# Kernel optimization log

Hardware: AMD Instinct MI355X
Metric: run time of the kernel (lower is better)

Reference implementation:

```python
import jax, jax.numpy as jnp
import numpy as np

B, P, H = 256, 20, 4  # images, boxes per image, humans per image
F, L, S, HD, C = 1024, 300, 16, 1024, 117

def _build_edges():
    s, d = np.meshgrid(np.arange(P), np.arange(P), indexing='ij')
    m = s != d
    src_l, dst_l = s[m], d[m]  # 380 fully-connected edges per image (src-major order)
    eid_tab = -np.ones((P, P), np.int64)
    eid_tab[src_l, dst_l] = np.arange(src_l.shape[0])
    rs, rd = np.meshgrid(np.arange(P), np.arange(H), indexing='ij')
    rm = rs != rd
    r_eid = eid_tab[rs[rm], rd[rm]]  # 76 readout edges per image (human dst)
    off_n = (np.arange(B) * P)[:, None]
    off_e = (np.arange(B) * src_l.shape[0])[:, None]
    edge_src = (src_l[None] + off_n).ravel().astype(np.int32)
    edge_dst = (dst_l[None] + off_n).ravel().astype(np.int32)
    readout_eid = (r_eid[None] + off_e).ravel().astype(np.int32)
    return edge_src, edge_dst, readout_eid

def setup_inputs() -> dict:
    key = jax.random.key(0)
    ks = jax.random.split(key, 12)
    es, ed, re = _build_edges()
    N = B * P
    D_in = 2 * F + 2 * L + S  # 2664
    return {
        'feat': jax.random.normal(ks[0], (N, F), jnp.float32),
        'word2vec': jax.random.normal(ks[1], (N, L), jnp.float32),
        'spatial_feat': jax.random.normal(ks[2], (es.shape[0], S), jnp.float32),
        'W_v': jax.random.normal(ks[3], (F, F), jnp.float32) / np.float32(np.sqrt(F)),
        'a_v': jax.random.normal(ks[4], (2 * F,), jnp.float32) * 0.05,
        'W_l': jax.random.normal(ks[5], (L, L), jnp.float32) / np.float32(np.sqrt(L)),
        'a_l': jax.random.normal(ks[6], (2 * L,), jnp.float32) * 0.05,
        'W1': jax.random.normal(ks[7], (D_in, HD), jnp.float32) / np.float32(np.sqrt(D_in)),
        'b1': jnp.zeros((HD,), jnp.float32),
        'W2': jax.random.normal(ks[8], (HD, C), jnp.float32) / np.float32(np.sqrt(HD)),
        'b2': jnp.zeros((C,), jnp.float32),
        'edge_src': jnp.asarray(es),
        'edge_dst': jnp.asarray(ed),
        'readout_eid': jnp.asarray(re),
    }

def _gat_update(x, W, a, src, dst, n):
    # graph-attention message passing (GRNN step): attention over incoming edges per dst
    h = x @ W                      # [N, d]
    d = h.shape[1]
    e_src = h @ a[:d]              # [N]
    e_dst = h @ a[d:]
    e = jax.nn.leaky_relu(e_src[src] + e_dst[dst], 0.2)          # [E]
    emax = jax.ops.segment_max(e, dst, num_segments=n)
    ee = jnp.exp(e - emax[dst])
    denom = jax.ops.segment_sum(ee, dst, num_segments=n)
    alpha = ee / (denom[dst] + 1e-9)                              # segment softmax
    msg = jax.ops.segment_sum(alpha[:, None] * h[src], dst, num_segments=n)  # [N, d]
    return jax.nn.relu(x + msg)

def reference(feat, word2vec, spatial_feat, W_v, a_v, W_l, a_l, W1, b1, W2, b2,
              edge_src, edge_dst, readout_eid):
    n = feat.shape[0]
    new_n_f = _gat_update(feat, W_v, a_v, edge_src, edge_dst, n)          # visual stream
    new_n_f_lang = _gat_update(word2vec, W_l, a_l, edge_src, edge_dst, n) # semantic stream
    s = edge_src[readout_eid]
    d = edge_dst[readout_eid]
    s_f = spatial_feat[readout_eid]
    # Predictor.forward: concat [dst visual, dst lang, edge spatial, src lang, src visual]
    x = jnp.concatenate([new_n_f[d], new_n_f_lang[d], s_f, new_n_f_lang[s], new_n_f[s]], axis=1)
    hdn = jax.nn.relu(x @ W1 + b1)
    return hdn @ W2 + b2  # [Er, 117] action logits
```

## Files before the change

### kernel.cpp

```cpp
#include <hip/hip_runtime.h>
#include <hip/hip_bf16.h>

#define BB 256
#define PP 20
#define HH 4
#define FF 1024
#define LL 300
#define LLP 320
#define DCAT 1344
#define SS 16
#define HDIM 1024
#define CC 117
#define NNODE (BB * PP)
#define NREAD (BB * (PP * HH - HH))
#define EPB 8
#define TK 32

typedef __attribute__((ext_vector_type(8))) short bf16x8v;
typedef __attribute__((ext_vector_type(4))) float f32x4v;
typedef __attribute__((ext_vector_type(4))) unsigned short u16x4;

__device__ __forceinline__ float bf2f(unsigned short u) {
  return __uint_as_float((unsigned int)u << 16);
}
__device__ __forceinline__ unsigned short f2b(float f) {
  __hip_bfloat16 h = __float2bfloat16(f);
  return *(unsigned short*)&h;
}

__global__ void sniff_dtype(const unsigned short* __restrict__ buf,
                            int* __restrict__ flag) {
  int t = threadIdx.x;
  int votes = 0;
  for (int i = t; i < 512; i += 256) {
    unsigned int u = (unsigned int)buf[i] << 16;
    float v = __uint_as_float(u);
    float a = fabsf(v);
    if (v == v && a > 9.3e-10f && a < 1.1e9f) votes++;
  }
  __shared__ int sv[256];
  sv[t] = votes;
  __syncthreads();
  for (int s = 128; s > 0; s >>= 1) {
    if (t < s) sv[t] += sv[t + s];
    __syncthreads();
  }
  if (t == 0) flag[0] = (sv[0] < 448) ? 1 : 0;
}

#define NB_FEAT 5120
#define NB_W2V 1600
#define NB_SM 79
#define PREP_BLOCKS 10739

__global__ __launch_bounds__(256) void prep_all(
    const void* __restrict__ s0, const void* __restrict__ s1,
    const void* __restrict__ s3, const void* __restrict__ s4,
    const void* __restrict__ s5, const void* __restrict__ s6,
    const void* __restrict__ s7, const void* __restrict__ s8,
    const void* __restrict__ s9, const void* __restrict__ s10,
    __hip_bfloat16* __restrict__ xcat, __hip_bfloat16* __restrict__ cAv,
    __hip_bfloat16* __restrict__ cAl, __hip_bfloat16* __restrict__ cB1,
    __hip_bfloat16* __restrict__ cB2, __hip_bfloat16* __restrict__ cW1sp,
    __hip_bfloat16* __restrict__ dWvT, __hip_bfloat16* __restrict__ dWlT,
    __hip_bfloat16* __restrict__ dW1d, __hip_bfloat16* __restrict__ dW1s,
    __hip_bfloat16* __restrict__ dW2T, const int* __restrict__ flag) {
  const int bid = blockIdx.x;
  const int t = threadIdx.x;
  const int fl = flag[0];

  if (bid < NB_FEAT) {
    long i = (long)bid * 256 + t;
    int r = (int)(i >> 8);
    int c = ((int)i & 255) * 4;
    u16x4 o;
    if (fl) {
      float4 v = *(const float4*)((const float*)s0 + (long)r * FF + c);
      o[0] = f2b(v.x); o[1] = f2b(v.y); o[2] = f2b(v.z); o[3] = f2b(v.w);
    } else {
      o = *(const u16x4*)((const __hip_bfloat16*)s0 + (long)r * FF + c);
    }
    *(u16x4*)(xcat + (long)r * DCAT + c) = o;
  } else if (bid < NB_FEAT + NB_W2V) {
    long i = (long)(bid - NB_FEAT) * 256 + t;
    int r = (int)(i / 80), c = ((int)(i % 80)) * 4;
    u16x4 o;
    if (c + 4 <= LL) {
      if (fl) {
        const float* p = (const float*)s1 + (long)r * LL + c;
        o[0] = f2b(p[0]); o[1] = f2b(p[1]); o[2] = f2b(p[2]); o[3] = f2b(p[3]);
      } else {
        const __hip_bfloat16* p = (const __hip_bfloat16*)s1 + (long)r * LL + c;
        o[0] = *(const unsigned short*)(p + 0);
        o[1] = *(const unsigned short*)(p + 1);
        o[2] = *(const unsigned short*)(p + 2);
        o[3] = *(const unsigned short*)(p + 3);
      }
    } else {
#pragma unroll
      for (int j = 0; j < 4; j++) {
        float v = 0.f;
        if (c + j < LL)
          v = fl ? ((const float*)s1)[(long)r * LL + c + j]
                 : __bfloat162float(
                       ((const __hip_bfloat16*)s1)[(long)r * LL + c + j]);
        o[j] = f2b(v);
      }
    }
    *(u16x4*)(xcat + (long)r * DCAT + FF + c) = o;
  } else if (bid < NB_FEAT + NB_W2V + NB_SM) {
    int i = (bid - NB_FEAT - NB_W2V) * 256 + t;
    auto rd = [&](const void* p, long idx) -> float {
      return fl ? ((const float*)p)[idx]
                : __bfloat162float(((const __hip_bfloat16*)p)[idx]);
    };
    if (i < 2048) cAv[i] = __float2bfloat16(rd(s4, i));
    else if (i < 2648) cAl[i - 2048] = __float2bfloat16(rd(s6, i - 2048));
    else if (i < 3672) cB1[i - 2648] = __float2bfloat16(rd(s8, i - 2648));
    else if (i < 3789) cB2[i - 3672] = __float2bfloat16(rd(s10, i - 3672));
    else if (i < 20173)
      cW1sp[i - 3789] = __float2bfloat16(rd(s7, 1355776L + (i - 3789)));
  } else {
    int idx = bid - (NB_FEAT + NB_W2V + NB_SM);
    const int OFFS[8] = {0, 1024, 1124, 2148, 2468, 3492, 3812, 3940};
    const int NKB[7] = {32, 10, 32, 10, 32, 10, 32};
    const int ROW0[7] = {0, 0, 0, 1024, 1640, 1340, 0};
    const int KK[7] = {1024, 300, 1024, 300, 1024, 300, 1024};
    const int NN[7] = {1024, 300, 1024, 1024, 1024, 1024, 117};
    const int LD[7] = {1024, 300, 1024, 1024, 1024, 1024, 117};
    const int KP[7] = {1024, 320, 1024, 320, 1024, 320, 1024};
    const int KOFF[7] = {0, 0, 0, 1024, 0, 1024, 0};
    const int KLD[7] = {1024, 320, DCAT, DCAT, DCAT, DCAT, 1024};
    int z = 0;
    while (z < 6 && idx >= OFFS[z + 1]) z++;
    idx -= OFFS[z];
    const int kb = (idx % NKB[z]) * 32, nb = (idx / NKB[z]) * 32;
    const void* src = (z == 0) ? s3 : (z == 1) ? s5 : (z == 6) ? s9 : s7;
    __hip_bfloat16* dst = (z == 0) ? dWvT : (z == 1) ? dWlT
                          : (z <= 3) ? dW1d : (z <= 5) ? dW1s : dW2T;
    const int row0 = ROW0[z], K = KK[z], N = NN[z], ld = LD[z], Kp = KP[z];
    const int koff = KOFF[z], kld = KLD[z];
    __shared__ float tile[32][33];
    const int tx = t & 31, ty = t >> 5;
    for (int i = ty; i < 32; i += 8) {
      int k = kb + i, n = nb + tx;
      float v = 0.f;
      if (k < K && n < N) {
        long sidx = (long)(row0 + k) * ld + n;
        v = fl ? ((const float*)src)[sidx]
               : __bfloat162float(((const __hip_bfloat16*)src)[sidx]);
      }
      tile[i][tx] = v;
    }
    __syncthreads();
    for (int i = ty; i < 32; i += 8) {
      int n = nb + i, k = kb + tx;
      if (n < N && k < Kp)
        dst[(long)n * kld + koff + k] = __float2bfloat16(tile[tx][i]);
    }
  }
}

struct GDesc {
  const __hip_bfloat16* A;
  const __hip_bfloat16* BT;
  void* C;
  const __hip_bfloat16* bias;
  int M, N, K, lda, ldbt, ldc;
  int row_mode, do_relu, c_mode, nbx, nby;
};

template <int BM, int BN, int WR, int WC>
__global__ __launch_bounds__(256) void gemm_db(GDesc d0, GDesc d1,
                                               const int* outflag) {
  constexpr int MI = BM / WR / 16;
  constexpr int NI = BN / WC / 16;
  __shared__ __hip_bfloat16 Asm[2][BM * TK];
  __shared__ __hip_bfloat16 Bsm[2][BN * TK];
  const GDesc d = blockIdx.z ? d1 : d0;
  if ((int)blockIdx.x >= d.nbx || (int)blockIdx.y >= d.nby) return;
  const int tid = threadIdx.x;
  const int lane = tid & 63;
  const int wave = tid >> 6;
  const int wm = (wave % WR) * (BM / WR);
  const int wn = (wave / WR) * (BN / WC);
  const int m0 = blockIdx.y * BM;
  const int n0 = blockIdx.x * BN;
  const int col_l = lane & 15;
  const int quad = lane >> 4;
  const __hip_bfloat16* A = d.A;
  const __hip_bfloat16* BT = d.BT;
  const int M = d.M, N = d.N, lda = d.lda, ldbt = d.ldbt;
  const int row_mode = d.row_mode;

  auto stage = [&](int k0, int buf) {
#pragma unroll
    for (int c = tid; c < BM * 4; c += 256) {
      int r = c >> 2;
      int koff = (c & 3) * 8;
      int row = m0 + r;
      if (row >= M) row = M - 1;
      long grow = row_mode ? ((long)(row >> 2) * PP + (row & 3)) : (long)row;
      const __hip_bfloat16* gp = A + grow * lda + k0 + koff;
      __builtin_amdgcn_global_load_lds(
          (const __attribute__((address_space(1))) unsigned int*)gp,
          (__attribute__((address_space(3))) unsigned int*)(&Asm[buf][c * 8]),
          16, 0, 0);
    }
#pragma unroll
    for (int c = tid; c < BN * 4; c += 256) {
      int r = c >> 2;
      int koff = (c & 3) * 8;
      int row = n0 + r;
      if (row >= N) row = N - 1;
      const __hip_bfloat16* gp = BT + (long)row * ldbt + k0 + koff;
      __builtin_amdgcn_global_load_lds(
          (const __attribute__((address_space(1))) unsigned int*)gp,
          (__attribute__((address_space(3))) unsigned int*)(&Bsm[buf][c * 8]),
          16, 0, 0);
    }
  };

  f32x4v acc[MI][NI];
#pragma unroll
  for (int i = 0; i < MI; i++)
#pragma unroll
    for (int j = 0; j < NI; j++)
#pragma unroll
      for (int r = 0; r < 4; r++) acc[i][j][r] = 0.f;

  const int nk = d.K / TK;
  stage(0, 0);
  __syncthreads();
  for (int kt = 0; kt < nk; kt++) {
    const int cur = kt & 1;
    if (kt + 1 < nk) stage((kt + 1) * TK, 1 - cur);
    bf16x8v af[MI], bfr[NI];
#pragma unroll
    for (int mi = 0; mi < MI; mi++)
      af[mi] =
          *(const bf16x8v*)&Asm[cur][(wm + mi * 16 + col_l) * TK + quad * 8];
#pragma unroll
    for (int ni = 0; ni < NI; ni++)
      bfr[ni] =
          *(const bf16x8v*)&Bsm[cur][(wn + ni * 16 + col_l) * TK + quad * 8];
#pragma unroll
    for (int mi = 0; mi < MI; mi++)
#pragma unroll
      for (int ni = 0; ni < NI; ni++)
        acc[mi][ni] = __builtin_amdgcn_mfma_f32_16x16x32_bf16(
            af[mi], bfr[ni], acc[mi][ni], 0, 0, 0);
    __syncthreads();
  }

  const int store_f32 =
      (d.c_mode == 1) || (d.c_mode == 2 && outflag && outflag[0]);
#pragma unroll
  for (int mi = 0; mi < MI; mi++) {
    int rbase = m0 + wm + mi * 16 + quad * 4;
#pragma unroll
    for (int ni = 0; ni < NI; ni++) {
      int col = n0 + wn + ni * 16 + col_l;
      if (col >= N) continue;
      float bv = d.bias ? __bfloat162float(d.bias[col]) : 0.f;
#pragma unroll
      for (int r = 0; r < 4; r++) {
        int row = rbase + r;
        if (row >= M) continue;
        float v = acc[mi][ni][r] + bv;
        if (d.do_relu) v = fmaxf(v, 0.f);
        if (store_f32)
          ((float*)d.C)[(long)row * d.ldc + col] = v;
        else
          ((__hip_bfloat16*)d.C)[(long)row * d.ldc + col] = __float2bfloat16(v);
      }
    }
  }
}

#define CHROW (DCAT / 4)

__global__ __launch_bounds__(1024) void attn_fused(
    const __hip_bfloat16* __restrict__ xcat,
    const __hip_bfloat16* __restrict__ hcat,
    const __hip_bfloat16* __restrict__ aV,
    const __hip_bfloat16* __restrict__ aL,
    __hip_bfloat16* __restrict__ newcat) {
  const int b = blockIdx.x;
  const int t = threadIdx.x;
  const long base = (long)b * PP * DCAT;

  __shared__ __hip_bfloat16 hs[PP][DCAT];
  __shared__ float esv[PP], edv[PP], esl[PP], edl[PP];
  __shared__ float alphaV[PP * PP], alphaL[PP * PP];

  for (int i = t; i < PP * CHROW; i += 1024) {
    int r = i / CHROW, c = (i % CHROW) * 4;
    *(u16x4*)&hs[r][c] = *(const u16x4*)(hcat + base + (long)r * DCAT + c);
  }
  __syncthreads();

  const int wave = t >> 6, lane = t & 63;
  for (int node = wave; node < PP; node += 16) {
    float s1 = 0.f, s2 = 0.f, s3 = 0.f, s4 = 0.f;
    for (int f = lane * 4; f < FF; f += 256) {
      u16x4 hv = *(const u16x4*)&hs[node][f];
      u16x4 a1 = *(const u16x4*)(aV + f);
      u16x4 a2 = *(const u16x4*)(aV + FF + f);
#pragma unroll
      for (int j = 0; j < 4; j++) {
        float hf = bf2f(hv[j]);
        s1 += hf * bf2f(a1[j]);
        s2 += hf * bf2f(a2[j]);
      }
    }
    for (int f = FF + lane * 4; f < FF + LL; f += 256) {
      u16x4 hv = *(const u16x4*)&hs[node][f];
      u16x4 a3 = *(const u16x4*)(aL + (f - FF));
      u16x4 a4 = *(const u16x4*)(aL + LL + (f - FF));
#pragma unroll
      for (int j = 0; j < 4; j++) {
        float hf = bf2f(hv[j]);
        s3 += hf * bf2f(a3[j]);
        s4 += hf * bf2f(a4[j]);
      }
    }
#pragma unroll
    for (int o = 32; o > 0; o >>= 1) {
      s1 += __shfl_down(s1, o);
      s2 += __shfl_down(s2, o);
      s3 += __shfl_down(s3, o);
      s4 += __shfl_down(s4, o);
    }
    if (lane == 0) {
      esv[node] = s1; edv[node] = s2; esl[node] = s3; edl[node] = s4;
    }
  }
  __syncthreads();

  if (t < 2 * PP) {
    const int strm = t / PP, dd = t % PP;
    const float* es = strm ? esl : esv;
    const float ed = strm ? edl[dd] : edv[dd];
    float lg[PP];
    float m = -1e30f;
#pragma unroll
    for (int s = 0; s < PP; s++) {
      float e;
      if (s == dd) e = -1e30f;
      else {
        float v = es[s] + ed;
        e = (v > 0.f) ? v : 0.2f * v;
      }
      lg[s] = e;
      m = fmaxf(m, e);
    }
    float sum = 0.f;
#pragma unroll
    for (int s = 0; s < PP; s++) {
      lg[s] = expf(lg[s] - m);
      sum += lg[s];
    }
    float inv = 1.f / (sum + 1e-9f);
    float* al = strm ? alphaL : alphaV;
#pragma unroll
    for (int s = 0; s < PP; s++) al[s * PP + dd] = lg[s] * inv;
  }
  __syncthreads();

  for (int i = t; i < PP * CHROW; i += 1024) {
    int dd = i / CHROW, c = (i % CHROW) * 4;
    u16x4 ov;
    if (c >= FF + LL) {
      ov[0] = 0; ov[1] = 0; ov[2] = 0; ov[3] = 0;
    } else {
      const float* al = (c < FF) ? (alphaV + dd) : (alphaL + dd);
      float a0 = 0.f, a1 = 0.f, a2 = 0.f, a3 = 0.f;
#pragma unroll
      for (int s = 0; s < PP; s++) {
        float w = al[s * PP];
        u16x4 hv = *(const u16x4*)&hs[s][c];
        a0 += w * bf2f(hv[0]);
        a1 += w * bf2f(hv[1]);
        a2 += w * bf2f(hv[2]);
        a3 += w * bf2f(hv[3]);
      }
      u16x4 xv = *(const u16x4*)(xcat + base + (long)dd * DCAT + c);
      ov[0] = f2b(fmaxf(bf2f(xv[0]) + a0, 0.f));
      ov[1] = f2b(fmaxf(bf2f(xv[1]) + a1, 0.f));
      ov[2] = f2b(fmaxf(bf2f(xv[2]) + a2, 0.f));
      ov[3] = f2b(fmaxf(bf2f(xv[3]) + a3, 0.f));
    }
    *(u16x4*)(newcat + base + (long)dd * DCAT + c) = ov;
  }
}

__global__ __launch_bounds__(256) void combine_kernel(
    const int* __restrict__ e_src, const int* __restrict__ e_dst,
    const int* __restrict__ r_eid, const void* __restrict__ spat_raw,
    const __hip_bfloat16* __restrict__ W1sp,
    const __hip_bfloat16* __restrict__ b1,
    const __hip_bfloat16* __restrict__ Yd, const __hip_bfloat16* __restrict__ Ys,
    __hip_bfloat16* __restrict__ hdn, const int* __restrict__ flag) {
  const int t = threadIdx.x;
  const int e0 = blockIdx.x * EPB;
  const int hd = t * 4;

  float w[SS][4];
#pragma unroll
  for (int k = 0; k < SS; k++) {
    u16x4 ww = *(const u16x4*)(W1sp + (long)k * HDIM + hd);
#pragma unroll
    for (int j = 0; j < 4; j++) w[k][j] = bf2f(ww[j]);
  }
  float bb[4];
  {
    u16x4 bv = *(const u16x4*)(b1 + hd);
#pragma unroll
    for (int j = 0; j < 4; j++) bb[j] = bf2f(bv[j]);
  }

  __shared__ int sh_s[EPB], sh_hx[EPB], sh_re[EPB];
  __shared__ float sh_sf[EPB][SS];
  if (t < EPB) {
    int re = r_eid[e0 + t];
    sh_re[t] = re;
    sh_s[t] = e_src[re];
    int d = e_dst[re];
    sh_hx[t] = (d / PP) * HH + (d % PP);
  }
  __syncthreads();
  if (t < EPB * SS) {
    int ee = t >> 4, k = t & 15;
    long idx = (long)sh_re[ee] * SS + k;
    sh_sf[ee][k] = flag[0]
                       ? ((const float*)spat_raw)[idx]
                       : __bfloat162float(((const __hip_bfloat16*)spat_raw)[idx]);
  }
  __syncthreads();

#pragma unroll
  for (int ee = 0; ee < EPB; ee++) {
    const int s = sh_s[ee];
    const int hx = sh_hx[ee];
    u16x4 yd = *(const u16x4*)(Yd + (long)hx * HDIM + hd);
    u16x4 ys = *(const u16x4*)(Ys + (long)s * HDIM + hd);
    float v[4];
#pragma unroll
    for (int j = 0; j < 4; j++) v[j] = bf2f(yd[j]) + bf2f(ys[j]) + bb[j];
#pragma unroll
    for (int k = 0; k < SS; k++) {
      float sfv = sh_sf[ee][k];
#pragma unroll
      for (int j = 0; j < 4; j++) v[j] += sfv * w[k][j];
    }
    u16x4 o;
#pragma unroll
    for (int j = 0; j < 4; j++) o[j] = f2b(fmaxf(v[j], 0.f));
    *(u16x4*)(hdn + (long)(e0 + ee) * HDIM + hd) = o;
  }
}

extern "C" void kernel_launch(void* const* d_in, const int* in_sizes, int n_in,
                              void* d_out, int out_size, void* d_ws,
                              size_t ws_size, hipStream_t stream) {
  const int* e_src = (const int*)d_in[11];
  const int* e_dst = (const int*)d_in[12];
  const int* r_eid = (const int*)d_in[13];
  (void)ws_size; (void)n_in; (void)in_sizes; (void)out_size;

  char* ws = (char*)d_ws;
  size_t off = 0;
  auto take = [&](size_t bytes) {
    char* p = ws + off;
    off += (bytes + 255) & ~(size_t)255;
    return p;
  };

  int* dflag = (int*)take(256);
  __hip_bfloat16* xcat   = (__hip_bfloat16*)take((size_t)NNODE * DCAT * 2);
  __hip_bfloat16* hcat   = (__hip_bfloat16*)take((size_t)NNODE * DCAT * 2);
  __hip_bfloat16* newcat = (__hip_bfloat16*)take((size_t)NNODE * DCAT * 2);
  __hip_bfloat16* cAv    = (__hip_bfloat16*)take((size_t)2 * FF * 2);
  __hip_bfloat16* cAl    = (__hip_bfloat16*)take((size_t)2 * LL * 2);
  __hip_bfloat16* cB1    = (__hip_bfloat16*)take((size_t)HDIM * 2);
  __hip_bfloat16* cB2    = (__hip_bfloat16*)take((size_t)CC * 2);
  __hip_bfloat16* cW1sp  = (__hip_bfloat16*)take((size_t)SS * HDIM * 2);
  __hip_bfloat16* WvT    = (__hip_bfloat16*)take((size_t)FF * FF * 2);
  __hip_bfloat16* WlT    = (__hip_bfloat16*)take((size_t)LL * LLP * 2);
  __hip_bfloat16* W1Td   = (__hip_bfloat16*)take((size_t)HDIM * DCAT * 2);
  __hip_bfloat16* W1Ts   = (__hip_bfloat16*)take((size_t)HDIM * DCAT * 2);
  __hip_bfloat16* W2T    = (__hip_bfloat16*)take((size_t)CC * HDIM * 2);
  __hip_bfloat16* Yd     = (__hip_bfloat16*)take((size_t)BB * HH * HDIM * 2);
  __hip_bfloat16* Ys     = (__hip_bfloat16*)take((size_t)NNODE * HDIM * 2);
  __hip_bfloat16* hdn    = (__hip_bfloat16*)take((size_t)NREAD * HDIM * 2);

  dim3 blk(256);

  sniff_dtype<<<1, blk, 0, stream>>>((const unsigned short*)d_in[0], dflag);

  prep_all<<<PREP_BLOCKS, blk, 0, stream>>>(
      d_in[0], d_in[1], d_in[3], d_in[4], d_in[5], d_in[6], d_in[7], d_in[8],
      d_in[9], d_in[10], xcat, cAv, cAl, cB1, cB2, cW1sp, WvT, WlT, W1Td, W1Ts,
      W2T, dflag);

  {
    GDesc pv{xcat, WvT, hcat, nullptr,
             NNODE, FF, FF, DCAT, FF, DCAT, 0, 0, 0, 8, 80};
    GDesc pl{xcat + FF, WlT, hcat + FF, nullptr,
             NNODE, LL, LLP, DCAT, LLP, DCAT, 0, 0, 0, 3, 80};
    gemm_db<64, 128, 2, 2><<<dim3(8, 80, 2), blk, 0, stream>>>(pv, pl,
                                                               nullptr);
  }

  attn_fused<<<BB, dim3(1024), 0, stream>>>(xcat, hcat, cAv, cAl, newcat);

  {
    GDesc gys{newcat, W1Ts, Ys, nullptr,
              NNODE, HDIM, DCAT, DCAT, DCAT, HDIM, 0, 0, 0, 8, 80};
    GDesc gyd{newcat, W1Td, Yd, nullptr,
              BB * HH, HDIM, DCAT, DCAT, DCAT, HDIM, 1, 0, 0, 8, 16};
    gemm_db<64, 128, 2, 2><<<dim3(8, 80, 2), blk, 0, stream>>>(gys, gyd,
                                                               nullptr);
  }

  combine_kernel<<<NREAD / EPB, blk, 0, stream>>>(e_src, e_dst, r_eid, d_in[2],
                                                  cW1sp, cB1, Yd, Ys, hdn,
                                                  dflag);

  {
    GDesc go{hdn, W2T, d_out, cB2,
             NREAD, CC, HDIM, HDIM, HDIM, CC, 0, 0, 2, 1, 608};
    gemm_db<32, 128, 1, 4><<<dim3(1, 608, 1), blk, 0, stream>>>(go, go, dflag);
  }
}
```

Baseline: 246.7 us.

## Replace LDS-staged GEMM with direct global-to-register fragment loads

The GEMM kernel no longer stages A/B tiles through double-buffered shared memory with global_load_lds and barriers. Each lane now loads its MFMA fragments straight from global memory into registers, prefetching the next k-step while the current one computes. This removes the LDS traffic and the per-iteration __syncthreads. In exchange, data shared between waves in a block is fetched redundantly from global memory or L2, and each 16-byte load is strided by the row pitch, which may lower coalescing.

Measured after the change: 374.4 us. 1.52x slower.

```diff
diff --git a/kernel.cpp b/kernel.cpp
--- a/kernel.cpp
+++ b/kernel.cpp
@@ -171,12 +171,10 @@
 };
 
 template <int BM, int BN, int WR, int WC>
-__global__ __launch_bounds__(256) void gemm_db(GDesc d0, GDesc d1,
-                                               const int* outflag) {
+__global__ __launch_bounds__(256) void gemm_direct(GDesc d0, GDesc d1,
+                                                   const int* outflag) {
   constexpr int MI = BM / WR / 16;
   constexpr int NI = BN / WC / 16;
-  __shared__ __hip_bfloat16 Asm[2][BM * TK];
-  __shared__ __hip_bfloat16 Bsm[2][BN * TK];
   const GDesc d = blockIdx.z ? d1 : d0;
   if ((int)blockIdx.x >= d.nbx || (int)blockIdx.y >= d.nby) return;
   const int tid = threadIdx.x;
@@ -188,38 +186,23 @@
   const int n0 = blockIdx.x * BN;
   const int col_l = lane & 15;
   const int quad = lane >> 4;
-  const __hip_bfloat16* A = d.A;
-  const __hip_bfloat16* BT = d.BT;
-  const int M = d.M, N = d.N, lda = d.lda, ldbt = d.ldbt;
-  const int row_mode = d.row_mode;
-
-  auto stage = [&](int k0, int buf) {
-#pragma unroll
-    for (int c = tid; c < BM * 4; c += 256) {
-      int r = c >> 2;
-      int koff = (c & 3) * 8;
-      int row = m0 + r;
-      if (row >= M) row = M - 1;
-      long grow = row_mode ? ((long)(row >> 2) * PP + (row & 3)) : (long)row;
-      const __hip_bfloat16* gp = A + grow * lda + k0 + koff;
-      __builtin_amdgcn_global_load_lds(
-          (const __attribute__((address_space(1))) unsigned int*)gp,
-          (__attribute__((address_space(3))) unsigned int*)(&Asm[buf][c * 8]),
-          16, 0, 0);
-    }
-#pragma unroll
-    for (int c = tid; c < BN * 4; c += 256) {
-      int r = c >> 2;
-      int koff = (c & 3) * 8;
-      int row = n0 + r;
-      if (row >= N) row = N - 1;
-      const __hip_bfloat16* gp = BT + (long)row * ldbt + k0 + koff;
-      __builtin_amdgcn_global_load_lds(
-          (const __attribute__((address_space(1))) unsigned int*)gp,
-          (__attribute__((address_space(3))) unsigned int*)(&Bsm[buf][c * 8]),
-          16, 0, 0);
-    }
-  };
+  const int M = d.M, N = d.N;
+
+  const __hip_bfloat16* pA[MI];
+#pragma unroll
+  for (int mi = 0; mi < MI; mi++) {
+    int row = m0 + wm + mi * 16 + col_l;
+    if (row >= M) row = M - 1;
+    long grow = d.row_mode ? ((long)(row >> 2) * PP + (row & 3)) : (long)row;
+    pA[mi] = d.A + grow * d.lda + quad * 8;
+  }
+  const __hip_bfloat16* pB[NI];
+#pragma unroll
+  for (int ni = 0; ni < NI; ni++) {
+    int row = n0 + wn + ni * 16 + col_l;
+    if (row >= N) row = N - 1;
+    pB[ni] = d.BT + (long)row * d.ldbt + quad * 8;
+  }
 
   f32x4v acc[MI][NI];
 #pragma unroll
@@ -230,27 +213,32 @@
       for (int r = 0; r < 4; r++) acc[i][j][r] = 0.f;
 
   const int nk = d.K / TK;
-  stage(0, 0);
-  __syncthreads();
+  bf16x8v afc[MI], bfc[NI], afn[MI], bfn[NI];
+#pragma unroll
+  for (int mi = 0; mi < MI; mi++) afc[mi] = *(const bf16x8v*)(pA[mi]);
+#pragma unroll
+  for (int ni = 0; ni < NI; ni++) bfc[ni] = *(const bf16x8v*)(pB[ni]);
+
   for (int kt = 0; kt < nk; kt++) {
-    const int cur = kt & 1;
-    if (kt + 1 < nk) stage((kt + 1) * TK, 1 - cur);
-    bf16x8v af[MI], bfr[NI];
-#pragma unroll
-    for (int mi = 0; mi < MI; mi++)
-      af[mi] =
-          *(const bf16x8v*)&Asm[cur][(wm + mi * 16 + col_l) * TK + quad * 8];
-#pragma unroll
-    for (int ni = 0; ni < NI; ni++)
-      bfr[ni] =
-          *(const bf16x8v*)&Bsm[cur][(wn + ni * 16 + col_l) * TK + quad * 8];
+    const int knext = (kt + 1) * TK;
+    if (kt + 1 < nk) {
+#pragma unroll
+      for (int mi = 0; mi < MI; mi++)
+        afn[mi] = *(const bf16x8v*)(pA[mi] + knext);
+#pragma unroll
+      for (int ni = 0; ni < NI; ni++)
+        bfn[ni] = *(const bf16x8v*)(pB[ni] + knext);
+    }
 #pragma unroll
     for (int mi = 0; mi < MI; mi++)
 #pragma unroll
       for (int ni = 0; ni < NI; ni++)
         acc[mi][ni] = __builtin_amdgcn_mfma_f32_16x16x32_bf16(
-            af[mi], bfr[ni], acc[mi][ni], 0, 0, 0);
-    __syncthreads();
+            afc[mi], bfc[ni], acc[mi][ni], 0, 0, 0);
+#pragma unroll
+    for (int mi = 0; mi < MI; mi++) afc[mi] = afn[mi];
+#pragma unroll
+    for (int ni = 0; ni < NI; ni++) bfc[ni] = bfn[ni];
   }
 
   const int store_f32 =
@@ -509,8 +497,8 @@
              NNODE, FF, FF, DCAT, FF, DCAT, 0, 0, 0, 8, 80};
     GDesc pl{xcat + FF, WlT, hcat + FF, nullptr,
              NNODE, LL, LLP, DCAT, LLP, DCAT, 0, 0, 0, 3, 80};
-    gemm_db<64, 128, 2, 2><<<dim3(8, 80, 2), blk, 0, stream>>>(pv, pl,
-                                                               nullptr);
+    gemm_direct<64, 128, 2, 2><<<dim3(8, 80, 2), blk, 0, stream>>>(pv, pl,
+                                                                   nullptr);
   }
 
   attn_fused<<<BB, dim3(1024), 0, stream>>>(xcat, hcat, cAv, cAl, newcat);
@@ -520,8 +508,8 @@
               NNODE, HDIM, DCAT, DCAT, DCAT, HDIM, 0, 0, 0, 8, 80};
     GDesc gyd{newcat, W1Td, Yd, nullptr,
               BB * HH, HDIM, DCAT, DCAT, DCAT, HDIM, 1, 0, 0, 8, 16};
-    gemm_db<64, 128, 2, 2><<<dim3(8, 80, 2), blk, 0, stream>>>(gys, gyd,
-                                                               nullptr);
+    gemm_direct<64, 128, 2, 2><<<dim3(8, 80, 2), blk, 0, stream>>>(gys, gyd,
+                                                                   nullptr);
   }
 
   combine_kernel<<<NREAD / EPB, blk, 0, stream>>>(e_src, e_dst, r_eid, d_in[2],
@@ -531,6 +519,7 @@
   {
     GDesc go{hdn, W2T, d_out, cB2,
              NREAD, CC, HDIM, HDIM, HDIM, CC, 0, 0, 2, 1, 608};
-    gemm_db<32, 128, 1, 4><<<dim3(1, 608, 1), blk, 0, stream>>>(go, go, dflag);
-  }
-}
+    gemm_direct<32, 128, 1, 4><<<dim3(1, 608, 1), blk, 0, stream>>>(go, go,
+                                                                    dflag);
+  }
+}
```
